# Performance work log

Measured on AMD Instinct MI355X. Metric: run time of the kernel, lower is better.

Reference implementation:

```python
import jax, jax.numpy as jnp
import numpy as np

B, S, D, F, E, K = 4, 2048, 1024, 4096, 8, 2
LBW = 0.01  # load_balance_weight


def setup_inputs() -> dict:
    key = jax.random.key(0)
    ks = jax.random.split(key, 8)
    sd, sf = 1.0 / np.sqrt(D), 1.0 / np.sqrt(F)
    return {
        "x": jax.random.normal(ks[0], (B, S, D), dtype=jnp.float32),
        "expert_weights": jax.random.normal(ks[1], (B, E), dtype=jnp.float32),
        "gate_w": jax.random.uniform(ks[2], (D, E), minval=-sd, maxval=sd),
        "gate_b": jnp.zeros((E,), jnp.float32),
        "w1": jax.random.uniform(ks[3], (E, D, F), minval=-sd, maxval=sd),
        "b1": jnp.zeros((E, F), jnp.float32),
        "w2": jax.random.uniform(ks[4], (E, F, D), minval=-sf, maxval=sf),
        "b2": jnp.zeros((E, D), jnp.float32),
    }


def reference(x, expert_weights, gate_w, gate_b, w1, b1, w2, b2):
    b, s, d = x.shape
    xf = x.reshape(-1, d)                       # (T, D), T = B*S
    T = xf.shape[0]

    logits = xf @ gate_w + gate_b               # (T, E)
    bias = jnp.broadcast_to(expert_weights[:, None, :], (b, s, E)).reshape(-1, E)
    gate_probs = jax.nn.softmax(logits + bias, axis=-1)

    topk_p, topk_i = jax.lax.top_k(gate_probs, K)
    topk_p = topk_p / topk_p.sum(axis=-1, keepdims=True)

    # combine[t, e] = renormalized routing weight of token t for expert e (0 if unrouted)
    combine = jnp.zeros((T, E), xf.dtype).at[jnp.arange(T)[:, None], topk_i].add(topk_p)

    out = jnp.zeros_like(xf)
    for e in range(E):  # fixed small expert loop; dense per-expert GEMMs (dropout inactive in eval)
        h = jax.nn.gelu(xf @ w1[e] + b1[e], approximate=False)  # torch GELU = exact erf
        out = out + combine[:, e:e + 1] * (h @ w2[e] + b2[e])

    # Switch-style load balance loss
    top1 = jnp.argmax(gate_probs, axis=-1)
    f = jnp.mean(jax.nn.one_hot(top1, E, dtype=gate_probs.dtype), axis=0)
    P = gate_probs.mean(axis=0)
    load_loss = LBW * E * jnp.sum(f * P)

    return out.reshape(b, s, d), load_loss
```

## Files before the change

### kernel.cpp

```cpp
#include <hip/hip_runtime.h>
#include <math.h>

#define B_ 4
#define S_ 2048
#define D_ 1024
#define F_ 4096
#define E_ 8
#define T_ 8192
#define LBW_ 0.01f
#define HROWS_ 17408

#define BUFB 49152
#define ABYTES 32768

typedef unsigned short u16;
typedef __attribute__((ext_vector_type(8))) short bf16x8;
typedef __attribute__((ext_vector_type(4))) float f32x4;

#define GLOAD16(gp, lp) __builtin_amdgcn_global_load_lds( \
    (const __attribute__((address_space(1))) void*)(gp),  \
    (__attribute__((address_space(3))) void*)(lp), 16, 0, 0)

__device__ __forceinline__ u16 f2b(float f) {
    unsigned u = __float_as_uint(f);
    u = (u + 0x7FFFu + ((u >> 16) & 1u)) >> 16;
    return (u16)u;
}
__device__ __forceinline__ float gelu_f(float v) {
    return 0.5f * v * (1.0f + erff(v * 0.70710678118654752440f));
}

__global__ __launch_bounds__(256) void cvt_T_kernel(const float* __restrict__ src,
                                                    u16* __restrict__ dst, int R, int C) {
    __shared__ u16 t[64][72];
    const int e = blockIdx.z;
    const float* s = src + (size_t)e * R * C;
    u16* d = dst + (size_t)e * R * C;
    const int r0 = blockIdx.y * 64, c0 = blockIdx.x * 64;
    const int tid = threadIdx.x;
    {
        int rr = tid >> 2, cq = (tid & 3) * 16;
        #pragma unroll
        for (int j = 0; j < 16; j += 4) {
            float4 v = *(const float4*)(s + (size_t)(r0 + rr) * C + c0 + cq + j);
            t[cq + j + 0][rr] = f2b(v.x);
            t[cq + j + 1][rr] = f2b(v.y);
            t[cq + j + 2][rr] = f2b(v.z);
            t[cq + j + 3][rr] = f2b(v.w);
        }
    }
    __syncthreads();
    {
        int cr = tid >> 2, rq = (tid & 3) * 16;
        #pragma unroll
        for (int j = 0; j < 16; j += 8) {
            int4 pk; u16* pw = (u16*)&pk;
            #pragma unroll
            for (int jj = 0; jj < 8; ++jj) pw[jj] = t[cr][rq + j + jj];
            *(int4*)(d + (size_t)(c0 + cr) * R + r0 + rq + j) = pk;
        }
    }
}

__global__ __launch_bounds__(64) void gate_kernel(
    const float* __restrict__ x, const float* __restrict__ ew,
    const float* __restrict__ gw, const float* __restrict__ gb,
    u16* __restrict__ xb,
    float* __restrict__ combine, int* __restrict__ idx, int* __restrict__ cnt,
    int* __restrict__ fcnt, float* __restrict__ psum)
{
    const int t = blockIdx.x, l = threadIdx.x;
    const float* xr = x + (size_t)t * D_;
    double acc[E_];
    #pragma unroll
    for (int e = 0; e < E_; ++e) acc[e] = 0.0;
    u16 xw[16];
    #pragma unroll
    for (int kk = 0; kk < 16; kk += 4) {
        float4 xv = *(const float4*)(xr + l * 16 + kk);
        float xs[4] = {xv.x, xv.y, xv.z, xv.w};
        #pragma unroll
        for (int j = 0; j < 4; ++j) {
            xw[kk + j] = f2b(xs[j]);
            const float* gr = gw + (size_t)(l * 16 + kk + j) * E_;
            float4 g0 = *(const float4*)(gr);
            float4 g1 = *(const float4*)(gr + 4);
            acc[0] += (double)xs[j] * g0.x;  acc[1] += (double)xs[j] * g0.y;
            acc[2] += (double)xs[j] * g0.z;  acc[3] += (double)xs[j] * g0.w;
            acc[4] += (double)xs[j] * g1.x;  acc[5] += (double)xs[j] * g1.y;
            acc[6] += (double)xs[j] * g1.z;  acc[7] += (double)xs[j] * g1.w;
        }
    }
    *(int4*)(xb + (size_t)t * D_ + l * 16)     = *(int4*)(xw);
    *(int4*)(xb + (size_t)t * D_ + l * 16 + 8) = *(int4*)(xw + 8);
    #pragma unroll
    for (int e = 0; e < E_; ++e) {
        #pragma unroll
        for (int m = 32; m > 0; m >>= 1) acc[e] += __shfl_xor(acc[e], m);
    }
    if (l == 0) {
        const int b = t / S_;
        double p[E_]; double mx = -1e300;
        #pragma unroll
        for (int e = 0; e < E_; ++e) {
            p[e] = acc[e] + (double)gb[e] + (double)ew[b * E_ + e];
            mx = fmax(mx, p[e]);
        }
        double s = 0.0;
        #pragma unroll
        for (int e = 0; e < E_; ++e) { p[e] = exp(p[e] - mx); s += p[e]; }
        double inv = 1.0 / s;
        #pragma unroll
        for (int e = 0; e < E_; ++e) p[e] *= inv;
        double m1 = -1.0; int e1 = 0;
        #pragma unroll
        for (int e = 0; e < E_; ++e) if (p[e] > m1) { m1 = p[e]; e1 = e; }
        double m2 = -1.0; int e2 = 0;
        #pragma unroll
        for (int e = 0; e < E_; ++e) if (e != e1 && p[e] > m2) { m2 = p[e]; e2 = e; }
        float c1 = (float)(m1 / (m1 + m2)), c2 = (float)(m2 / (m1 + m2));
        #pragma unroll
        for (int e = 0; e < E_; ++e)
            combine[t * E_ + e] = (e == e1) ? c1 : ((e == e2) ? c2 : 0.0f);
        int q1 = atomicAdd(&cnt[e1], 1); idx[e1 * T_ + q1] = t;
        int q2 = atomicAdd(&cnt[e2], 1); idx[e2 * T_ + q2] = t;
        atomicAdd(&fcnt[(t & 63) * E_ + e1], 1);
        #pragma unroll
        for (int e = 0; e < E_; ++e) atomicAdd(&psum[(t & 63) * E_ + e], (float)p[e]);
    }
}

__global__ void offsets_kernel(const int* __restrict__ cnt, int* __restrict__ off) {
    if (threadIdx.x == 0 && blockIdx.x == 0) {
        int o = 0;
        for (int e = 0; e < E_; ++e) { off[e] = o; o += ((cnt[e] + 127) >> 7) << 7; }
    }
}

template<int NT, bool IS_G1>
__global__ __launch_bounds__(512, 2) void moe_gemm_kernel(
    const u16* __restrict__ Aglob, const u16* __restrict__ Wt,
    const float* __restrict__ bias, const float* __restrict__ combine,
    const int* __restrict__ idxAll, const int* __restrict__ cntAll,
    const int* __restrict__ off,
    u16* __restrict__ hOut, float* __restrict__ out)
{
    constexpr int KD = NT * 64;
    const int e = blockIdx.z;
    const int cnt = cntAll[e];
    const int tm = blockIdx.y, tn = blockIdx.x;
    if (tm * 256 >= cnt) return;
    const int base = off[e];
    const int* idx_e = idxAll + e * T_;
    const u16* Bsrc = Wt + (size_t)e * ((size_t)D_ * F_);

    __shared__ __align__(16) char ldsr[3 * BUFB];

    const int tid = threadIdx.x;
    const int l = tid & 63, wid = tid >> 6;
    const int wm = (wid >> 1) * 64, wn = (wid & 1) * 64;
    const int lr = l & 15, lg = l >> 4;

    const int lrow8 = l >> 3;
    const int schunk = (l & 7) ^ lrow8;
    const u16* aptr[4]; const u16* bptr[2];
    #pragma unroll
    for (int i = 0; i < 4; ++i) {
        int row = (i * 8 + wid) * 8 + lrow8;
        int r = tm * 256 + row;
        if (IS_G1) {
            int tok = (r < cnt) ? idx_e[r] : idx_e[0];
            aptr[i] = Aglob + (size_t)tok * KD + schunk * 8;
        } else {
            int hr = base + r; if (hr > HROWS_ - 1) hr = HROWS_ - 1;
            aptr[i] = Aglob + (size_t)hr * KD + schunk * 8;
        }
    }
    #pragma unroll
    for (int j = 0; j < 2; ++j) {
        int row = (j * 8 + wid) * 8 + lrow8;
        bptr[j] = Bsrc + (size_t)(tn * 128 + row) * KD + schunk * 8;
    }

    f32x4 acc[4][4];
    #pragma unroll
    for (int mi = 0; mi < 4; ++mi)
        #pragma unroll
        for (int ni = 0; ni < 4; ++ni)
            acc[mi][ni] = (f32x4){0.f, 0.f, 0.f, 0.f};

    auto stage = [&](int sb, int kofe) {
        #pragma unroll
        for (int i = 0; i < 4; ++i)
            GLOAD16(aptr[i] + kofe, ldsr + sb + (i * 8 + wid) * 1024);
        #pragma unroll
        for (int j = 0; j < 2; ++j)
            GLOAD16(bptr[j] + kofe, ldsr + sb + ABYTES + (j * 8 + wid) * 1024);
    };

    stage(0, 0);
    stage(BUFB, 64);
    asm volatile("s_waitcnt vmcnt(6)" ::: "memory");
    __builtin_amdgcn_s_barrier();

    int cb = 0, sb2 = 2 * BUFB;
    int kofe = 128;
    for (int t = 0; t < NT; ++t) {
        bf16x8 af[8], bfv[8];
        #pragma unroll
        for (int kb = 0; kb < 2; ++kb)
            #pragma unroll
            for (int mi = 0; mi < 4; ++mi) {
                int row = wm + mi * 16 + lr;
                af[kb * 4 + mi] = *(const bf16x8*)(ldsr + cb + row * 128 + (((kb * 4 + lg) ^ (lr & 7)) * 16));
            }
        #pragma unroll
        for (int kb = 0; kb < 2; ++kb)
            #pragma unroll
            for (int ni = 0; ni < 4; ++ni) {
                int row = wn + ni * 16 + lr;
                bfv[kb * 4 + ni] = *(const bf16x8*)(ldsr + cb + ABYTES + row * 128 + (((kb * 4 + lg) ^ (lr & 7)) * 16));
            }
        if (t < NT - 2) { stage(sb2, kofe); kofe += 64; }
        __builtin_amdgcn_s_setprio(1);
        #pragma unroll
        for (int kb = 0; kb < 2; ++kb)
            #pragma unroll
            for (int mi = 0; mi < 4; ++mi)
                #pragma unroll
                for (int ni = 0; ni < 4; ++ni)
                    acc[mi][ni] = __builtin_amdgcn_mfma_f32_16x16x32_bf16(af[kb * 4 + mi], bfv[kb * 4 + ni], acc[mi][ni], 0, 0, 0);
        __builtin_amdgcn_s_setprio(0);
        if (t < NT - 2)       { asm volatile("s_waitcnt vmcnt(6)" ::: "memory"); }
        else if (t == NT - 2) { asm volatile("s_waitcnt vmcnt(0)" ::: "memory"); }
        if (t < NT - 1) __builtin_amdgcn_s_barrier();
        cb += BUFB;  if (cb == 3 * BUFB)  cb = 0;
        sb2 += BUFB; if (sb2 == 3 * BUFB) sb2 = 0;
    }

    if (IS_G1) {
        const float* be = bias + e * F_;
        const int pad = ((cnt + 127) >> 7) << 7;
        #pragma unroll
        for (int mi = 0; mi < 4; ++mi) {
            #pragma unroll
            for (int j = 0; j < 4; ++j) {
                int rl = tm * 256 + wm + mi * 16 + lg * 4 + j;
                if (rl < pad) {
                    size_t srow = (size_t)(base + rl) * F_;
                    #pragma unroll
                    for (int ni = 0; ni < 4; ++ni) {
                        int f = tn * 128 + wn + ni * 16 + lr;
                        hOut[srow + f] = f2b(gelu_f(acc[mi][ni][j] + be[f]));
                    }
                }
            }
        }
    } else {
        const float* be = bias + e * D_;
        #pragma unroll
        for (int mi = 0; mi < 4; ++mi) {
            #pragma unroll
            for (int j = 0; j < 4; ++j) {
                int rl = tm * 256 + wm + mi * 16 + lg * 4 + j;
                if (rl < cnt) {
                    int tkn = idx_e[rl];
                    float cw = combine[tkn * E_ + e];
                    float* orow = out + (size_t)tkn * D_;
                    #pragma unroll
                    for (int ni = 0; ni < 4; ++ni) {
                        int d = tn * 128 + wn + ni * 16 + lr;
                        atomicAdd(&orow[d], cw * (acc[mi][ni][j] + be[d]));
                    }
                }
            }
        }
    }
}

__global__ void loss_kernel(const int* __restrict__ fcnt, const float* __restrict__ psum,
                            float* __restrict__ dst) {
    if (threadIdx.x == 0 && blockIdx.x == 0) {
        float loss = 0.f;
        for (int e = 0; e < E_; ++e) {
            float fs = 0.f, Ps = 0.f;
            for (int s = 0; s < 64; ++s) { fs += (float)fcnt[s * E_ + e]; Ps += psum[s * E_ + e]; }
            loss += (fs / (float)T_) * (Ps / (float)T_);
        }
        *dst = LBW_ * (float)E_ * loss;
    }
}

__global__ void sentinel_kernel(float* __restrict__ dst) {
    if (threadIdx.x == 0) dst[0] = -12345.0f;
}

extern "C" void kernel_launch(void* const* d_in, const int* in_sizes, int n_in,
                              void* d_out, int out_size, void* d_ws, size_t ws_size,
                              hipStream_t stream)
{
    const float* x  = (const float*)d_in[0];
    const float* ew = (const float*)d_in[1];
    const float* gw = (const float*)d_in[2];
    const float* gb = (const float*)d_in[3];
    const float* w1 = (const float*)d_in[4];
    const float* b1 = (const float*)d_in[5];
    const float* w2 = (const float*)d_in[6];
    const float* b2 = (const float*)d_in[7];
    float* out = (float*)d_out;

    char* ws = (char*)d_ws;
    size_t o = 0;
    u16* w1t = (u16*)(ws + o); o += (size_t)E_ * D_ * F_ * 2;
    u16* w2t = (u16*)(ws + o); o += (size_t)E_ * F_ * D_ * 2;
    u16* xb  = (u16*)(ws + o); o += (size_t)T_ * D_ * 2;
    u16* h   = (u16*)(ws + o); o += (size_t)HROWS_ * F_ * 2;
    float* combine = (float*)(ws + o); o += (size_t)T_ * E_ * 4;
    int* idx = (int*)(ws + o); o += (size_t)E_ * T_ * 4;
    size_t zoff = o;
    int* cnt   = (int*)(ws + o); o += 128;
    int* fcnt  = (int*)(ws + o); o += 64 * E_ * 4;
    float* psum = (float*)(ws + o); o += 64 * E_ * 4;
    int* off   = (int*)(ws + o); o += 128;
    const size_t ws_needed = o;

    if (ws_size < ws_needed) {
        hipMemsetAsync(d_out, 0, (size_t)out_size * sizeof(float), stream);
        sentinel_kernel<<<1, 64, 0, stream>>>(out + (size_t)out_size - 1);
        return;
    }

    hipMemsetAsync(ws + zoff, 0, ws_needed - zoff, stream);
    hipMemsetAsync(d_out, 0, (size_t)out_size * sizeof(float), stream);

    cvt_T_kernel<<<dim3(F_ / 64, D_ / 64, E_), 256, 0, stream>>>(w1, w1t, D_, F_);
    cvt_T_kernel<<<dim3(D_ / 64, F_ / 64, E_), 256, 0, stream>>>(w2, w2t, F_, D_);
    gate_kernel<<<T_, 64, 0, stream>>>(x, ew, gw, gb, xb, combine, idx, cnt, fcnt, psum);
    offsets_kernel<<<1, 64, 0, stream>>>(cnt, off);
    moe_gemm_kernel<16, true><<<dim3(F_ / 128, T_ / 256, E_), 512, 0, stream>>>(
        xb, w1t, b1, nullptr, idx, cnt, off, h, nullptr);
    moe_gemm_kernel<64, false><<<dim3(D_ / 128, T_ / 256, E_), 512, 0, stream>>>(
        h, w2t, b2, combine, idx, cnt, off, nullptr, out);
    loss_kernel<<<1, 64, 0, stream>>>(fcnt, psum, out + (size_t)out_size - 1);
}
```

Measured before the change: 857.4 us.

## Switch MoE GEMM to 256x256 tiles with K=32 stages and expert-interleaved grid

Reshapes the MoE expert GEMM from 256x128 output tiles with 64-wide K steps to 256x256 tiles with 32-wide K steps. Each wave now computes a 128x64 sub-tile, and the LDS swizzle and load mapping are rewritten to match. The 3-D grid is flattened into 1-D with the expert index in the low bits, so consecutive blocks belong to different experts. The larger tile is meant to raise arithmetic intensity and cut redundant A/B global reads. In exchange it uses more accumulator registers, gives fewer MFMAs per barrier, and launches fewer blocks.

```diff
diff --git a/kernel.cpp b/kernel.cpp
--- a/kernel.cpp
+++ b/kernel.cpp
@@ -10,8 +10,8 @@
 #define LBW_ 0.01f
 #define HROWS_ 17408
 
-#define BUFB 49152
-#define ABYTES 32768
+#define BUFB 32768
+#define ABYTES 16384
 
 typedef unsigned short u16;
 typedef __attribute__((ext_vector_type(8))) short bf16x8;
@@ -145,10 +145,12 @@
     const int* __restrict__ off,
     u16* __restrict__ hOut, float* __restrict__ out)
 {
-    constexpr int KD = NT * 64;
-    const int e = blockIdx.z;
+    constexpr int KD = NT * 32;
+    const int gid = blockIdx.x;
+    const int e = gid & 7;
+    const int tm = (gid >> 3) & 31;
+    const int tn = gid >> 8;
     const int cnt = cntAll[e];
-    const int tm = blockIdx.y, tn = blockIdx.x;
     if (tm * 256 >= cnt) return;
     const int base = off[e];
     const int* idx_e = idxAll + e * T_;
@@ -158,80 +160,66 @@
 
     const int tid = threadIdx.x;
     const int l = tid & 63, wid = tid >> 6;
-    const int wm = (wid >> 1) * 64, wn = (wid & 1) * 64;
-    const int lr = l & 15, lg = l >> 4;
-
-    const int lrow8 = l >> 3;
-    const int schunk = (l & 7) ^ lrow8;
-    const u16* aptr[4]; const u16* bptr[2];
-    #pragma unroll
-    for (int i = 0; i < 4; ++i) {
-        int row = (i * 8 + wid) * 8 + lrow8;
+    const int wm = (wid >> 2) * 128, wn = (wid & 3) * 64;
+    const int lr = l & 15, lg = (l >> 4) & 3;
+
+    const int lrow = l >> 2;
+    const int cS8 = (((l & 3) ^ ((l >> 2) & 3) ^ ((l >> 4) & 3)) << 3);
+    const u16* aptr[2]; const u16* bptr[2];
+    #pragma unroll
+    for (int i = 0; i < 2; ++i) {
+        int row = i * 128 + wid * 16 + lrow;
         int r = tm * 256 + row;
         if (IS_G1) {
             int tok = (r < cnt) ? idx_e[r] : idx_e[0];
-            aptr[i] = Aglob + (size_t)tok * KD + schunk * 8;
+            aptr[i] = Aglob + (size_t)tok * KD + cS8;
         } else {
             int hr = base + r; if (hr > HROWS_ - 1) hr = HROWS_ - 1;
-            aptr[i] = Aglob + (size_t)hr * KD + schunk * 8;
-        }
-    }
-    #pragma unroll
-    for (int j = 0; j < 2; ++j) {
-        int row = (j * 8 + wid) * 8 + lrow8;
-        bptr[j] = Bsrc + (size_t)(tn * 128 + row) * KD + schunk * 8;
-    }
-
-    f32x4 acc[4][4];
-    #pragma unroll
-    for (int mi = 0; mi < 4; ++mi)
+            aptr[i] = Aglob + (size_t)hr * KD + cS8;
+        }
+        bptr[i] = Bsrc + (size_t)(tn * 256 + row) * KD + cS8;
+    }
+    const int wof = wid * 1024;
+
+    f32x4 acc[8][4];
+    #pragma unroll
+    for (int mi = 0; mi < 8; ++mi)
         #pragma unroll
         for (int ni = 0; ni < 4; ++ni)
             acc[mi][ni] = (f32x4){0.f, 0.f, 0.f, 0.f};
 
     auto stage = [&](int sb, int kofe) {
-        #pragma unroll
-        for (int i = 0; i < 4; ++i)
-            GLOAD16(aptr[i] + kofe, ldsr + sb + (i * 8 + wid) * 1024);
-        #pragma unroll
-        for (int j = 0; j < 2; ++j)
-            GLOAD16(bptr[j] + kofe, ldsr + sb + ABYTES + (j * 8 + wid) * 1024);
+        GLOAD16(aptr[0] + kofe, ldsr + sb + wof);
+        GLOAD16(aptr[1] + kofe, ldsr + sb + wof + 8192);
+        GLOAD16(bptr[0] + kofe, ldsr + sb + ABYTES + wof);
+        GLOAD16(bptr[1] + kofe, ldsr + sb + ABYTES + wof + 8192);
     };
 
     stage(0, 0);
-    stage(BUFB, 64);
-    asm volatile("s_waitcnt vmcnt(6)" ::: "memory");
+    stage(BUFB, 32);
+    asm volatile("s_waitcnt vmcnt(4)" ::: "memory");
     __builtin_amdgcn_s_barrier();
 
+    const int koff = ((lg ^ (lr & 3) ^ ((lr >> 2) & 3)) << 4);
     int cb = 0, sb2 = 2 * BUFB;
-    int kofe = 128;
+    int kofe = 64;
     for (int t = 0; t < NT; ++t) {
-        bf16x8 af[8], bfv[8];
-        #pragma unroll
-        for (int kb = 0; kb < 2; ++kb)
+        bf16x8 af[8], bfv[4];
+        #pragma unroll
+        for (int mi = 0; mi < 8; ++mi)
+            af[mi] = *(const bf16x8*)(ldsr + cb + (wm + mi * 16 + lr) * 64 + koff);
+        #pragma unroll
+        for (int ni = 0; ni < 4; ++ni)
+            bfv[ni] = *(const bf16x8*)(ldsr + cb + ABYTES + (wn + ni * 16 + lr) * 64 + koff);
+        if (t < NT - 2) { stage(sb2, kofe); kofe += 32; }
+        __builtin_amdgcn_s_setprio(1);
+        #pragma unroll
+        for (int mi = 0; mi < 8; ++mi)
             #pragma unroll
-            for (int mi = 0; mi < 4; ++mi) {
-                int row = wm + mi * 16 + lr;
-                af[kb * 4 + mi] = *(const bf16x8*)(ldsr + cb + row * 128 + (((kb * 4 + lg) ^ (lr & 7)) * 16));
-            }
-        #pragma unroll
-        for (int kb = 0; kb < 2; ++kb)
-            #pragma unroll
-            for (int ni = 0; ni < 4; ++ni) {
-                int row = wn + ni * 16 + lr;
-                bfv[kb * 4 + ni] = *(const bf16x8*)(ldsr + cb + ABYTES + row * 128 + (((kb * 4 + lg) ^ (lr & 7)) * 16));
-            }
-        if (t < NT - 2) { stage(sb2, kofe); kofe += 64; }
-        __builtin_amdgcn_s_setprio(1);
-        #pragma unroll
-        for (int kb = 0; kb < 2; ++kb)
-            #pragma unroll
-            for (int mi = 0; mi < 4; ++mi)
-                #pragma unroll
-                for (int ni = 0; ni < 4; ++ni)
-                    acc[mi][ni] = __builtin_amdgcn_mfma_f32_16x16x32_bf16(af[kb * 4 + mi], bfv[kb * 4 + ni], acc[mi][ni], 0, 0, 0);
+            for (int ni = 0; ni < 4; ++ni)
+                acc[mi][ni] = __builtin_amdgcn_mfma_f32_16x16x32_bf16(af[mi], bfv[ni], acc[mi][ni], 0, 0, 0);
         __builtin_amdgcn_s_setprio(0);
-        if (t < NT - 2)       { asm volatile("s_waitcnt vmcnt(6)" ::: "memory"); }
+        if (t < NT - 2)       { asm volatile("s_waitcnt vmcnt(4)" ::: "memory"); }
         else if (t == NT - 2) { asm volatile("s_waitcnt vmcnt(0)" ::: "memory"); }
         if (t < NT - 1) __builtin_amdgcn_s_barrier();
         cb += BUFB;  if (cb == 3 * BUFB)  cb = 0;
@@ -242,7 +230,7 @@
         const float* be = bias + e * F_;
         const int pad = ((cnt + 127) >> 7) << 7;
         #pragma unroll
-        for (int mi = 0; mi < 4; ++mi) {
+        for (int mi = 0; mi < 8; ++mi) {
             #pragma unroll
             for (int j = 0; j < 4; ++j) {
                 int rl = tm * 256 + wm + mi * 16 + lg * 4 + j;
@@ -250,7 +238,7 @@
                     size_t srow = (size_t)(base + rl) * F_;
                     #pragma unroll
                     for (int ni = 0; ni < 4; ++ni) {
-                        int f = tn * 128 + wn + ni * 16 + lr;
+                        int f = tn * 256 + wn + ni * 16 + lr;
                         hOut[srow + f] = f2b(gelu_f(acc[mi][ni][j] + be[f]));
                     }
                 }
@@ -259,7 +247,7 @@
     } else {
         const float* be = bias + e * D_;
         #pragma unroll
-        for (int mi = 0; mi < 4; ++mi) {
+        for (int mi = 0; mi < 8; ++mi) {
             #pragma unroll
             for (int j = 0; j < 4; ++j) {
                 int rl = tm * 256 + wm + mi * 16 + lg * 4 + j;
@@ -269,7 +257,7 @@
                     float* orow = out + (size_t)tkn * D_;
                     #pragma unroll
                     for (int ni = 0; ni < 4; ++ni) {
-                        int d = tn * 128 + wn + ni * 16 + lr;
+                        int d = tn * 256 + wn + ni * 16 + lr;
                         atomicAdd(&orow[d], cw * (acc[mi][ni][j] + be[d]));
                     }
                 }
@@ -337,9 +325,9 @@
     cvt_T_kernel<<<dim3(D_ / 64, F_ / 64, E_), 256, 0, stream>>>(w2, w2t, F_, D_);
     gate_kernel<<<T_, 64, 0, stream>>>(x, ew, gw, gb, xb, combine, idx, cnt, fcnt, psum);
     offsets_kernel<<<1, 64, 0, stream>>>(cnt, off);
-    moe_gemm_kernel<16, true><<<dim3(F_ / 128, T_ / 256, E_), 512, 0, stream>>>(
+    moe_gemm_kernel<32, true><<<8 * 32 * (F_ / 256), 512, 0, stream>>>(
         xb, w1t, b1, nullptr, idx, cnt, off, h, nullptr);
-    moe_gemm_kernel<64, false><<<dim3(D_ / 128, T_ / 256, E_), 512, 0, stream>>>(
+    moe_gemm_kernel<128, false><<<8 * 32 * (D_ / 256), 512, 0, stream>>>(
         h, w2t, b2, combine, idx, cnt, off, nullptr, out);
     loss_kernel<<<1, 64, 0, stream>>>(fcnt, psum, out + (size_t)out_size - 1);
 }
```

New measurement: 1.104 ms. 28.8% more time.

## Use 256x256 MoE GEMM tiles with a compact tile table and 8-wave pipeline

Applied to the files above, without the earlier changes.

Replaces the 256x128 grouped GEMM with a 256x256 tile per 512-thread block, split into four quadrant phases with double-buffered LDS and interleaved B/A staging between barriers. A tile table built after gating lists only the occupied (expert, row-tile) pairs, so the 1D grid launches no empty blocks, and block ids are remapped to spread work across XCDs. The larger tile halves operand reloads per FLOP. In exchange it uses 128KB of LDS and 128 accumulator registers per thread, which can lower occupancy, and adds more barriers per k-step.

```diff
diff --git a/kernel.cpp b/kernel.cpp
--- a/kernel.cpp
+++ b/kernel.cpp
@@ -9,9 +9,7 @@
 #define T_ 8192
 #define LBW_ 0.01f
 #define HROWS_ 17408
-
-#define BUFB 49152
-#define ABYTES 32768
+#define NTILE_MAX 72
 
 typedef unsigned short u16;
 typedef __attribute__((ext_vector_type(8))) short bf16x8;
@@ -20,6 +18,9 @@
 #define GLOAD16(gp, lp) __builtin_amdgcn_global_load_lds( \
     (const __attribute__((address_space(1))) void*)(gp),  \
     (__attribute__((address_space(3))) void*)(lp), 16, 0, 0)
+
+#define MEMBAR() asm volatile("" ::: "memory")
+#define BARRIER() do { MEMBAR(); __builtin_amdgcn_s_barrier(); MEMBAR(); } while (0)
 
 __device__ __forceinline__ u16 f2b(float f) {
     unsigned u = __float_as_uint(f);
@@ -130,127 +131,196 @@
     }
 }
 
-__global__ void offsets_kernel(const int* __restrict__ cnt, int* __restrict__ off) {
+__global__ void tiletab_kernel(const int* __restrict__ cnt, int* __restrict__ off,
+                               int* __restrict__ table, int* __restrict__ ntab) {
     if (threadIdx.x == 0 && blockIdx.x == 0) {
-        int o = 0;
-        for (int e = 0; e < E_; ++e) { off[e] = o; o += ((cnt[e] + 127) >> 7) << 7; }
-    }
-}
-
-template<int NT, bool IS_G1>
-__global__ __launch_bounds__(512, 2) void moe_gemm_kernel(
+        int o = 0, k = 0;
+        for (int e = 0; e < E_; ++e) {
+            off[e] = o;
+            int pad = ((cnt[e] + 127) >> 7) << 7;
+            o += pad;
+            int nt = (pad + 255) >> 8;
+            for (int i = 0; i < nt; ++i) table[k++] = e | (i << 4);
+        }
+        *ntab = k;
+    }
+}
+
+template<int NT, int NTN, bool IS_G1>
+__global__ __launch_bounds__(512, 2) void moe_gemm8(
     const u16* __restrict__ Aglob, const u16* __restrict__ Wt,
     const float* __restrict__ bias, const float* __restrict__ combine,
     const int* __restrict__ idxAll, const int* __restrict__ cntAll,
-    const int* __restrict__ off,
+    const int* __restrict__ off, const int* __restrict__ table,
+    const int* __restrict__ ntab,
     u16* __restrict__ hOut, float* __restrict__ out)
 {
     constexpr int KD = NT * 64;
-    const int e = blockIdx.z;
-    const int cnt = cntAll[e];
-    const int tm = blockIdx.y, tn = blockIdx.x;
-    if (tm * 256 >= cnt) return;
-    const int base = off[e];
+    constexpr int NWG = NTILE_MAX * NTN;
+    const int gid2 = ((int)blockIdx.x & 7) * (NWG >> 3) + ((int)blockIdx.x >> 3);
+    const int tn = gid2 / NTILE_MAX;
+    const int ti = gid2 % NTILE_MAX;
+    if (ti >= *ntab) return;
+    const int ent = table[ti];
+    const int e = ent & 15, tm = ent >> 4;
+    const int cnt = cntAll[e], base = off[e];
     const int* idx_e = idxAll + e * T_;
     const u16* Bsrc = Wt + (size_t)e * ((size_t)D_ * F_);
 
-    __shared__ __align__(16) char ldsr[3 * BUFB];
+    __shared__ __align__(16) char lds[131072];
 
     const int tid = threadIdx.x;
     const int l = tid & 63, wid = tid >> 6;
-    const int wm = (wid >> 1) * 64, wn = (wid & 1) * 64;
+    const int h = wid >> 2, g = wid & 3;
     const int lr = l & 15, lg = l >> 4;
 
-    const int lrow8 = l >> 3;
-    const int schunk = (l & 7) ^ lrow8;
-    const u16* aptr[4]; const u16* bptr[2];
+    const int rl = wid * 8 + (l >> 3);
+    const int sk8 = (((l & 7) ^ ((l >> 3) & 7)) << 3);
+    const u16* aP[4]; const u16* bP[4];
+    {
+        const int crow[4] = { rl, 128 + rl, 64 + rl, 192 + rl };
+        #pragma unroll
+        for (int c = 0; c < 4; ++c) {
+            int r = tm * 256 + crow[c];
+            if (IS_G1) {
+                int tok = (r < cnt) ? idx_e[r] : idx_e[0];
+                aP[c] = Aglob + (size_t)tok * KD + sk8;
+            } else {
+                int hr = base + r; if (hr > HROWS_ - 1) hr = HROWS_ - 1;
+                aP[c] = Aglob + (size_t)hr * KD + sk8;
+            }
+        }
+        const int g2 = rl >> 5, o5 = rl & 31;
+        const int ccol[4] = { g2 * 64 + o5,      (2 + g2) * 64 + o5,
+                              g2 * 64 + 32 + o5, (2 + g2) * 64 + 32 + o5 };
+        #pragma unroll
+        for (int c = 0; c < 4; ++c)
+            bP[c] = Bsrc + (size_t)(tn * 256 + ccol[c]) * KD + sk8;
+    }
+    const int sdst = wid * 1024;
+
+    f32x4 acc[8][4];
     #pragma unroll
-    for (int i = 0; i < 4; ++i) {
-        int row = (i * 8 + wid) * 8 + lrow8;
-        int r = tm * 256 + row;
-        if (IS_G1) {
-            int tok = (r < cnt) ? idx_e[r] : idx_e[0];
-            aptr[i] = Aglob + (size_t)tok * KD + schunk * 8;
-        } else {
-            int hr = base + r; if (hr > HROWS_ - 1) hr = HROWS_ - 1;
-            aptr[i] = Aglob + (size_t)hr * KD + schunk * 8;
-        }
-    }
-    #pragma unroll
-    for (int j = 0; j < 2; ++j) {
-        int row = (j * 8 + wid) * 8 + lrow8;
-        bptr[j] = Bsrc + (size_t)(tn * 128 + row) * KD + schunk * 8;
-    }
-
-    f32x4 acc[4][4];
-    #pragma unroll
-    for (int mi = 0; mi < 4; ++mi)
-        #pragma unroll
-        for (int ni = 0; ni < 4; ++ni)
-            acc[mi][ni] = (f32x4){0.f, 0.f, 0.f, 0.f};
-
-    auto stage = [&](int sb, int kofe) {
-        #pragma unroll
-        for (int i = 0; i < 4; ++i)
-            GLOAD16(aptr[i] + kofe, ldsr + sb + (i * 8 + wid) * 1024);
-        #pragma unroll
-        for (int j = 0; j < 2; ++j)
-            GLOAD16(bptr[j] + kofe, ldsr + sb + ABYTES + (j * 8 + wid) * 1024);
+    for (int mi = 0; mi < 8; ++mi)
+        #pragma unroll
+        for (int ni = 0; ni < 4; ++ni) acc[mi][ni] = (f32x4){0.f,0.f,0.f,0.f};
+
+    auto stageA = [&](int c, int buf, int kof) {
+        GLOAD16(aP[c] + kof, lds + buf * 65536 + c * 8192 + sdst);
     };
-
-    stage(0, 0);
-    stage(BUFB, 64);
+    auto stageB = [&](int c, int buf, int kof) {
+        GLOAD16(bP[c] + kof, lds + buf * 65536 + 32768 + c * 8192 + sdst);
+    };
+
+    stageA(0,0,0); stageA(1,0,0);
+    stageB(0,0,0); stageB(1,0,0); stageB(2,0,0); stageB(3,0,0);
+    stageA(2,0,0); stageA(3,0,0);
+    stageA(0,1,64); stageA(1,1,64);
     asm volatile("s_waitcnt vmcnt(6)" ::: "memory");
-    __builtin_amdgcn_s_barrier();
-
-    int cb = 0, sb2 = 2 * BUFB;
-    int kofe = 128;
+    BARRIER();
+
+    const int koff0 = ((lg ^ (lr & 7)) << 4);
+    bf16x8 a[8], blo[4], bhi[4];
+
     for (int t = 0; t < NT; ++t) {
-        bf16x8 af[8], bfv[8];
+        const int cb = (t & 1) * 65536;
+        const int nbuf = (t + 1) & 1;
+        const int kof1 = (t + 1) * 64, kof2 = (t + 2) * 64;
+        #pragma unroll
+        for (int kb = 0; kb < 2; ++kb) {
+            const int ko = koff0 ^ (kb << 6);
+            #pragma unroll
+            for (int mi = 0; mi < 4; ++mi)
+                a[kb*4+mi] = *(const bf16x8*)(lds + cb + (h*64 + mi*16 + lr)*128 + ko);
+            #pragma unroll
+            for (int ni = 0; ni < 2; ++ni)
+                blo[kb*2+ni] = *(const bf16x8*)(lds + cb + 32768 + (g*32 + ni*16 + lr)*128 + ko);
+        }
+        if (t + 1 < NT) { stageB(0, nbuf, kof1); stageB(1, nbuf, kof1); }
+        if (t == NT - 1) asm volatile("s_waitcnt vmcnt(2)" ::: "memory");
+        else             asm volatile("s_waitcnt vmcnt(6)" ::: "memory");
+        BARRIER();
+        __builtin_amdgcn_s_setprio(1);
         #pragma unroll
         for (int kb = 0; kb < 2; ++kb)
             #pragma unroll
-            for (int mi = 0; mi < 4; ++mi) {
-                int row = wm + mi * 16 + lr;
-                af[kb * 4 + mi] = *(const bf16x8*)(ldsr + cb + row * 128 + (((kb * 4 + lg) ^ (lr & 7)) * 16));
-            }
+            for (int mi = 0; mi < 4; ++mi)
+                #pragma unroll
+                for (int ni = 0; ni < 2; ++ni)
+                    acc[mi][ni] = __builtin_amdgcn_mfma_f32_16x16x32_bf16(a[kb*4+mi], blo[kb*2+ni], acc[mi][ni], 0,0,0);
+        __builtin_amdgcn_s_setprio(0);
+        BARRIER();
+        #pragma unroll
+        for (int kb = 0; kb < 2; ++kb) {
+            const int ko = koff0 ^ (kb << 6);
+            #pragma unroll
+            for (int ni = 0; ni < 2; ++ni)
+                bhi[kb*2+ni] = *(const bf16x8*)(lds + cb + 32768 + (128 + g*32 + ni*16 + lr)*128 + ko);
+        }
+        if (t + 1 < NT) { stageB(2, nbuf, kof1); stageB(3, nbuf, kof1); }
+        if (t == NT - 1) asm volatile("s_waitcnt vmcnt(0)" ::: "memory");
+        else             asm volatile("s_waitcnt vmcnt(6)" ::: "memory");
+        BARRIER();
+        __builtin_amdgcn_s_setprio(1);
         #pragma unroll
         for (int kb = 0; kb < 2; ++kb)
             #pragma unroll
-            for (int ni = 0; ni < 4; ++ni) {
-                int row = wn + ni * 16 + lr;
-                bfv[kb * 4 + ni] = *(const bf16x8*)(ldsr + cb + ABYTES + row * 128 + (((kb * 4 + lg) ^ (lr & 7)) * 16));
-            }
-        if (t < NT - 2) { stage(sb2, kofe); kofe += 64; }
+            for (int mi = 0; mi < 4; ++mi)
+                #pragma unroll
+                for (int ni = 0; ni < 2; ++ni)
+                    acc[mi][2+ni] = __builtin_amdgcn_mfma_f32_16x16x32_bf16(a[kb*4+mi], bhi[kb*2+ni], acc[mi][2+ni], 0,0,0);
+        __builtin_amdgcn_s_setprio(0);
+        BARRIER();
+        #pragma unroll
+        for (int kb = 0; kb < 2; ++kb) {
+            const int ko = koff0 ^ (kb << 6);
+            #pragma unroll
+            for (int mi = 0; mi < 4; ++mi)
+                a[kb*4+mi] = *(const bf16x8*)(lds + cb + (128 + h*64 + mi*16 + lr)*128 + ko);
+        }
+        if (t + 1 < NT) { stageA(2, nbuf, kof1); stageA(3, nbuf, kof1); }
+        if (t < NT - 1)  asm volatile("s_waitcnt vmcnt(6)" ::: "memory");
+        BARRIER();
         __builtin_amdgcn_s_setprio(1);
         #pragma unroll
         for (int kb = 0; kb < 2; ++kb)
             #pragma unroll
             for (int mi = 0; mi < 4; ++mi)
                 #pragma unroll
-                for (int ni = 0; ni < 4; ++ni)
-                    acc[mi][ni] = __builtin_amdgcn_mfma_f32_16x16x32_bf16(af[kb * 4 + mi], bfv[kb * 4 + ni], acc[mi][ni], 0, 0, 0);
+                for (int ni = 0; ni < 2; ++ni)
+                    acc[4+mi][ni] = __builtin_amdgcn_mfma_f32_16x16x32_bf16(a[kb*4+mi], blo[kb*2+ni], acc[4+mi][ni], 0,0,0);
         __builtin_amdgcn_s_setprio(0);
-        if (t < NT - 2)       { asm volatile("s_waitcnt vmcnt(6)" ::: "memory"); }
-        else if (t == NT - 2) { asm volatile("s_waitcnt vmcnt(0)" ::: "memory"); }
-        if (t < NT - 1) __builtin_amdgcn_s_barrier();
-        cb += BUFB;  if (cb == 3 * BUFB)  cb = 0;
-        sb2 += BUFB; if (sb2 == 3 * BUFB) sb2 = 0;
-    }
-
+        BARRIER();
+        if (t + 2 < NT)      { stageA(0, t & 1, kof2); stageA(1, t & 1, kof2); }
+        if (t == NT - 2)      asm volatile("s_waitcnt vmcnt(4)" ::: "memory");
+        else if (t < NT - 2)  asm volatile("s_waitcnt vmcnt(6)" ::: "memory");
+        BARRIER();
+        __builtin_amdgcn_s_setprio(1);
+        #pragma unroll
+        for (int kb = 0; kb < 2; ++kb)
+            #pragma unroll
+            for (int mi = 0; mi < 4; ++mi)
+                #pragma unroll
+                for (int ni = 0; ni < 2; ++ni)
+                    acc[4+mi][2+ni] = __builtin_amdgcn_mfma_f32_16x16x32_bf16(a[kb*4+mi], bhi[kb*2+ni], acc[4+mi][2+ni], 0,0,0);
+        __builtin_amdgcn_s_setprio(0);
+        BARRIER();
+    }
+
+    const int wm = h * 128, wn = g * 64;
     if (IS_G1) {
         const float* be = bias + e * F_;
         const int pad = ((cnt + 127) >> 7) << 7;
         #pragma unroll
-        for (int mi = 0; mi < 4; ++mi) {
+        for (int mi = 0; mi < 8; ++mi) {
             #pragma unroll
             for (int j = 0; j < 4; ++j) {
-                int rl = tm * 256 + wm + mi * 16 + lg * 4 + j;
-                if (rl < pad) {
-                    size_t srow = (size_t)(base + rl) * F_;
+                int rl2 = tm * 256 + wm + mi * 16 + lg * 4 + j;
+                if (rl2 < pad) {
+                    size_t srow = (size_t)(base + rl2) * F_;
                     #pragma unroll
                     for (int ni = 0; ni < 4; ++ni) {
-                        int f = tn * 128 + wn + ni * 16 + lr;
+                        int f = tn * 256 + wn + ni * 16 + lr;
                         hOut[srow + f] = f2b(gelu_f(acc[mi][ni][j] + be[f]));
                     }
                 }
@@ -259,17 +329,17 @@
     } else {
         const float* be = bias + e * D_;
         #pragma unroll
-        for (int mi = 0; mi < 4; ++mi) {
+        for (int mi = 0; mi < 8; ++mi) {
             #pragma unroll
             for (int j = 0; j < 4; ++j) {
-                int rl = tm * 256 + wm + mi * 16 + lg * 4 + j;
-                if (rl < cnt) {
-                    int tkn = idx_e[rl];
+                int rl2 = tm * 256 + wm + mi * 16 + lg * 4 + j;
+                if (rl2 < cnt) {
+                    int tkn = idx_e[rl2];
                     float cw = combine[tkn * E_ + e];
                     float* orow = out + (size_t)tkn * D_;
                     #pragma unroll
                     for (int ni = 0; ni < 4; ++ni) {
-                        int d = tn * 128 + wn + ni * 16 + lr;
+                        int d = tn * 256 + wn + ni * 16 + lr;
                         atomicAdd(&orow[d], cw * (acc[mi][ni][j] + be[d]));
                     }
                 }
@@ -322,6 +392,8 @@
     int* fcnt  = (int*)(ws + o); o += 64 * E_ * 4;
     float* psum = (float*)(ws + o); o += 64 * E_ * 4;
     int* off   = (int*)(ws + o); o += 128;
+    int* table = (int*)(ws + o); o += 512;
+    int* ntab  = (int*)(ws + o); o += 128;
     const size_t ws_needed = o;
 
     if (ws_size < ws_needed) {
@@ -336,10 +408,10 @@
     cvt_T_kernel<<<dim3(F_ / 64, D_ / 64, E_), 256, 0, stream>>>(w1, w1t, D_, F_);
     cvt_T_kernel<<<dim3(D_ / 64, F_ / 64, E_), 256, 0, stream>>>(w2, w2t, F_, D_);
     gate_kernel<<<T_, 64, 0, stream>>>(x, ew, gw, gb, xb, combine, idx, cnt, fcnt, psum);
-    offsets_kernel<<<1, 64, 0, stream>>>(cnt, off);
-    moe_gemm_kernel<16, true><<<dim3(F_ / 128, T_ / 256, E_), 512, 0, stream>>>(
-        xb, w1t, b1, nullptr, idx, cnt, off, h, nullptr);
-    moe_gemm_kernel<64, false><<<dim3(D_ / 128, T_ / 256, E_), 512, 0, stream>>>(
-        h, w2t, b2, combine, idx, cnt, off, nullptr, out);
+    tiletab_kernel<<<1, 64, 0, stream>>>(cnt, off, table, ntab);
+    moe_gemm8<16, 16, true><<<NTILE_MAX * 16, 512, 0, stream>>>(
+        xb, w1t, b1, nullptr, idx, cnt, off, table, ntab, h, nullptr);
+    moe_gemm8<64, 4, false><<<NTILE_MAX * 4, 512, 0, stream>>>(
+        h, w2t, b2, combine, idx, cnt, off, table, ntab, nullptr, out);
     loss_kernel<<<1, 64, 0, stream>>>(fcnt, psum, out + (size_t)out_size - 1);
 }
```

After: 896.7 us. 4.6% more time.
